# Performance work log

Measured on AMD Instinct MI355X. Metric: run time of the kernel, lower is better.

Reference implementation:

```python
import jax, jax.numpy as jnp
import numpy as np
from jax import lax

D_MODEL = 1024
D_STATE = 16
D_CONV = 4
D_INNER = 2048  # d_model * expand
B = 1
L = 1024


def setup_inputs() -> dict:
    key = jax.random.key(0)
    ks = jax.random.split(key, 8)
    nrm = lambda k, shape, s: jax.random.normal(k, shape, jnp.float32) * s
    x = nrm(ks[0], (B, L, D_MODEL), 1.0)
    in_proj_w = nrm(ks[1], (2 * D_INNER, D_MODEL), D_MODEL ** -0.5)
    conv_w = nrm(ks[2], (D_INNER, 1, D_CONV), D_CONV ** -0.5)
    conv_b = nrm(ks[3], (D_INNER,), 0.02)
    x_proj_w = nrm(ks[4], (D_INNER + 4 * D_STATE, D_INNER), D_INNER ** -0.5)
    # small dt so the log-cumsum-exp scan stays finite in fp32 over L steps
    dt_proj_w = nrm(ks[5], (D_INNER, D_INNER), 0.01 * D_INNER ** -0.5)
    dt_proj_b = jnp.full((D_INNER,), -6.0, jnp.float32)
    # faithful A_log init: real = -0.5*log(n), imag = pi*n
    n = np.arange(1, D_STATE + 1, dtype=np.float32)
    A_log_re = jnp.asarray(np.tile(np.log(n) * -0.5, (D_INNER, 1)))
    A_log_im = jnp.asarray(np.tile(np.pi * n, (D_INNER, 1)))
    D = jnp.ones((D_INNER,), jnp.float32)
    out_proj_w = nrm(ks[6], (D_MODEL, D_INNER), D_INNER ** -0.5)
    return dict(x=x, in_proj_w=in_proj_w, conv_w=conv_w, conv_b=conv_b,
                x_proj_w=x_proj_w, dt_proj_w=dt_proj_w, dt_proj_b=dt_proj_b,
                A_log_re=A_log_re, A_log_im=A_log_im, D=D, out_proj_w=out_proj_w)


def reference(x, in_proj_w, conv_w, conv_b, x_proj_w, dt_proj_w, dt_proj_b,
              A_log_re, A_log_im, D, out_proj_w):
    # input projection and gate split
    xz = x @ in_proj_w.T                          # (B, L, 2*d_inner)
    xc, z = jnp.split(xz, 2, axis=-1)
    # causal depthwise conv1d (torch pads both sides then truncates -> left pad only)
    xt = jnp.transpose(xc, (0, 2, 1))             # (B, d_inner, L)
    xp = jnp.pad(xt, ((0, 0), (0, 0), (D_CONV - 1, 0)))
    conv = lax.conv_general_dilated(
        xp, conv_w, window_strides=(1,), padding='VALID',
        dimension_numbers=('NCH', 'OIH', 'NCH'),
        feature_group_count=D_INNER) + conv_b[None, :, None]
    u = jnp.transpose(jax.nn.silu(conv), (0, 2, 1))  # (B, L, d_inner)
    # ssm parameter projection
    ssm = u @ x_proj_w.T                          # (B, L, d_inner + 4*d_state)
    delta = ssm[..., :D_INNER]
    B_re = ssm[..., D_INNER:D_INNER + D_STATE]
    B_im = ssm[..., D_INNER + D_STATE:D_INNER + 2 * D_STATE]
    C_re = ssm[..., D_INNER + 2 * D_STATE:D_INNER + 3 * D_STATE]
    C_im = ssm[..., D_INNER + 3 * D_STATE:]
    delta = jax.nn.softplus(delta @ dt_proj_w.T + dt_proj_b)  # (B, L, d_inner)
    Bc = (B_re + 1j * B_im).astype(jnp.complex64)             # (B, L, d_state)
    Cc = (C_re + 1j * C_im).astype(jnp.complex64)
    # complex selective scan via bilinear (Cayley) discretization + log-cumsum-exp
    A = -jnp.exp((A_log_re + 1j * A_log_im).astype(jnp.complex64))  # (d_inner, d_state)
    dt_c = delta[..., None].astype(jnp.complex64)             # (B, L, d_inner, 1)
    denom = 2.0 - dt_c * A                                    # (B, L, d_inner, d_state)
    numer = 2.0 + dt_c * A
    log_A_bar = jnp.log(numer) - jnp.log(denom)
    u_bar = (2.0 * dt_c / denom) * Bc[:, :, None, :] * u[..., None].astype(jnp.complex64)
    lc = jnp.cumsum(log_A_bar, axis=1)                        # cumulative log transition
    H = jnp.cumsum(jnp.exp(-lc) * u_bar, axis=1) * jnp.exp(lc)
    y = jnp.sum(Cc[:, :, None, :] * H, axis=-1).real + D * u  # (B, L, d_inner)
    y = y * jax.nn.silu(z)
    return y @ out_proj_w.T                                   # (B, L, d_model)
```

## Files before the change

kernel.cpp:

```cpp
#include <hip/hip_runtime.h>
#include <hip/hip_bf16.h>
#include <math.h>

#define L_SEQ   1024
#define DMODEL  1024
#define DINNER  2048
#define DSTATE  16
#define DCONV   4
#define NPROJ   (DINNER + 4 * DSTATE)
#define NCHUNK  16
#define CHUNK   64
#define NDN     (DINNER * DSTATE)

typedef __attribute__((ext_vector_type(8))) short  short8;
typedef __attribute__((ext_vector_type(8))) unsigned short us8;
typedef __attribute__((ext_vector_type(4))) float  f32x4;
typedef __attribute__((ext_vector_type(4))) unsigned short us4;

__device__ __forceinline__ float softplus_f(float v) {
    return fmaxf(v, 0.f) + log1pf(expf(-fabsf(v)));
}
__device__ __forceinline__ float silu_f(float v) {
    return v * __builtin_amdgcn_rcpf(1.f + expf(-v));
}

__device__ __forceinline__ void split1(float x, unsigned short& h, unsigned short& l) {
    unsigned b  = __float_as_uint(x);
    unsigned hb = b & 0xffff0000u;
    float    r  = x - __uint_as_float(hb);
    unsigned rb = __float_as_uint(r) + 0x8000u;
    h = (unsigned short)(hb >> 16);
    l = (unsigned short)(rb >> 16);
}
__device__ __forceinline__ void split4(float4 v, us4& h, us4& l) {
    float vv[4] = {v.x, v.y, v.z, v.w};
    #pragma unroll
    for (int i = 0; i < 4; ++i) {
        unsigned b  = __float_as_uint(vv[i]);
        unsigned hb = b & 0xffff0000u;
        float    r  = vv[i] - __uint_as_float(hb);
        unsigned rb = __float_as_uint(r) + 0x8000u;
        h[i] = (unsigned short)(hb >> 16);
        l[i] = (unsigned short)(rb >> 16);
    }
}

template<int BM>
__global__ __launch_bounds__(256) void gemm_mfma_sk(
    const float* __restrict__ A, const float* __restrict__ W,
    float* __restrict__ Cp, int M, int N, int K, int lda)
{
    constexpr int MF = BM / 32;
    constexpr int NF = 2;
    __shared__ unsigned short sAh[BM * 40], sAl[BM * 40];
    __shared__ unsigned short sBh[64 * 40], sBl[64 * 40];

    const int tid  = threadIdx.x;
    const int w    = tid >> 6;
    const int lane = tid & 63;
    const int wr   = w >> 1;
    const int wc   = w & 1;
    const int lrow = lane & 15;
    const int lkb  = lane >> 4;
    const int row0 = blockIdx.y * BM;
    const int col0 = blockIdx.x * 64;

    const int KS   = K / gridDim.z;
    const int kbeg = blockIdx.z * KS;
    const int kend = kbeg + KS;

    const int srow = tid >> 3;
    const int sfq  = tid & 7;

    f32x4 acc[MF][NF];
    #pragma unroll
    for (int m = 0; m < MF; ++m)
        #pragma unroll
        for (int n = 0; n < NF; ++n)
            acc[m][n] = (f32x4){0.f, 0.f, 0.f, 0.f};

    for (int k0 = kbeg; k0 < kend; k0 += 32) {
        #pragma unroll
        for (int p = 0; p < BM / 32; ++p) {
            int r = srow + p * 32;
            float4 v = *reinterpret_cast<const float4*>(
                A + (size_t)(row0 + r) * lda + k0 + sfq * 4);
            us4 h, l;
            split4(v, h, l);
            *reinterpret_cast<us4*>(sAh + r * 40 + sfq * 4) = h;
            *reinterpret_cast<us4*>(sAl + r * 40 + sfq * 4) = l;
        }
        #pragma unroll
        for (int p = 0; p < 2; ++p) {
            int r = srow + p * 32;
            float4 v = *reinterpret_cast<const float4*>(
                W + (size_t)(col0 + r) * K + k0 + sfq * 4);
            us4 h, l;
            split4(v, h, l);
            *reinterpret_cast<us4*>(sBh + r * 40 + sfq * 4) = h;
            *reinterpret_cast<us4*>(sBl + r * 40 + sfq * 4) = l;
        }
        __syncthreads();

        short8 ah[MF], al[MF], bh[NF], bl[NF];
        #pragma unroll
        for (int m = 0; m < MF; ++m) {
            int off = (wr * (BM / 2) + m * 16 + lrow) * 40 + lkb * 8;
            ah[m] = *reinterpret_cast<const short8*>(sAh + off);
            al[m] = *reinterpret_cast<const short8*>(sAl + off);
        }
        #pragma unroll
        for (int n = 0; n < NF; ++n) {
            int off = (wc * 32 + n * 16 + lrow) * 40 + lkb * 8;
            bh[n] = *reinterpret_cast<const short8*>(sBh + off);
            bl[n] = *reinterpret_cast<const short8*>(sBl + off);
        }

        #pragma unroll
        for (int m = 0; m < MF; ++m)
            #pragma unroll
            for (int n = 0; n < NF; ++n) {
                acc[m][n] = __builtin_amdgcn_mfma_f32_16x16x32_bf16(
                    ah[m], bh[n], acc[m][n], 0, 0, 0);
                acc[m][n] = __builtin_amdgcn_mfma_f32_16x16x32_bf16(
                    ah[m], bl[n], acc[m][n], 0, 0, 0);
                acc[m][n] = __builtin_amdgcn_mfma_f32_16x16x32_bf16(
                    al[m], bh[n], acc[m][n], 0, 0, 0);
            }
        __syncthreads();
    }

    float* Cb = Cp + (size_t)blockIdx.z * M * N;
    #pragma unroll
    for (int m = 0; m < MF; ++m)
        #pragma unroll
        for (int n = 0; n < NF; ++n) {
            int gr0 = row0 + wr * (BM / 2) + m * 16 + lkb * 4;
            int gc  = col0 + wc * 32 + n * 16 + lrow;
            #pragma unroll
            for (int r = 0; r < 4; ++r)
                Cb[(size_t)(gr0 + r) * N + gc] = acc[m][n][r];
        }
}

template<int BM>
__global__ __launch_bounds__(256) void gemm_bf16a_sk(
    const unsigned short* __restrict__ Ah, const unsigned short* __restrict__ Al,
    const float* __restrict__ W, float* __restrict__ Cp, int M, int N, int K)
{
    constexpr int MF = BM / 32;
    constexpr int NF = 2;
    constexpr int NL = BM / 64;
    __shared__ unsigned short sAh[BM * 40], sAl[BM * 40];
    __shared__ unsigned short sBh[64 * 40], sBl[64 * 40];

    const int tid  = threadIdx.x;
    const int w    = tid >> 6;
    const int lane = tid & 63;
    const int wr   = w >> 1;
    const int wc   = w & 1;
    const int lrow = lane & 15;
    const int lkb  = lane >> 4;
    const int row0 = blockIdx.y * BM;
    const int col0 = blockIdx.x * 64;

    const int KS   = K / gridDim.z;
    const int kbeg = blockIdx.z * KS;
    const int kend = kbeg + KS;

    const int srow = tid >> 3;
    const int sfq  = tid & 7;

    f32x4 acc[MF][NF];
    #pragma unroll
    for (int m = 0; m < MF; ++m)
        #pragma unroll
        for (int n = 0; n < NF; ++n)
            acc[m][n] = (f32x4){0.f, 0.f, 0.f, 0.f};

    for (int k0 = kbeg; k0 < kend; k0 += 32) {
        #pragma unroll
        for (int j = 0; j < NL; ++j) {
            int idx8 = j * 256 + tid;
            int r    = idx8 >> 2;
            int kq   = (idx8 & 3) * 8;
            size_t g = (size_t)(row0 + r) * K + k0 + kq;
            *reinterpret_cast<us8*>(sAh + r * 40 + kq) =
                *reinterpret_cast<const us8*>(Ah + g);
            *reinterpret_cast<us8*>(sAl + r * 40 + kq) =
                *reinterpret_cast<const us8*>(Al + g);
        }
        #pragma unroll
        for (int p = 0; p < 2; ++p) {
            int r = srow + p * 32;
            float4 v = *reinterpret_cast<const float4*>(
                W + (size_t)(col0 + r) * K + k0 + sfq * 4);
            us4 h, l;
            split4(v, h, l);
            *reinterpret_cast<us4*>(sBh + r * 40 + sfq * 4) = h;
            *reinterpret_cast<us4*>(sBl + r * 40 + sfq * 4) = l;
        }
        __syncthreads();

        short8 ah[MF], al[MF], bh[NF], bl[NF];
        #pragma unroll
        for (int m = 0; m < MF; ++m) {
            int off = (wr * (BM / 2) + m * 16 + lrow) * 40 + lkb * 8;
            ah[m] = *reinterpret_cast<const short8*>(sAh + off);
            al[m] = *reinterpret_cast<const short8*>(sAl + off);
        }
        #pragma unroll
        for (int n = 0; n < NF; ++n) {
            int off = (wc * 32 + n * 16 + lrow) * 40 + lkb * 8;
            bh[n] = *reinterpret_cast<const short8*>(sBh + off);
            bl[n] = *reinterpret_cast<const short8*>(sBl + off);
        }

        #pragma unroll
        for (int m = 0; m < MF; ++m)
            #pragma unroll
            for (int n = 0; n < NF; ++n) {
                acc[m][n] = __builtin_amdgcn_mfma_f32_16x16x32_bf16(
                    ah[m], bh[n], acc[m][n], 0, 0, 0);
                acc[m][n] = __builtin_amdgcn_mfma_f32_16x16x32_bf16(
                    ah[m], bl[n], acc[m][n], 0, 0, 0);
                acc[m][n] = __builtin_amdgcn_mfma_f32_16x16x32_bf16(
                    al[m], bh[n], acc[m][n], 0, 0, 0);
            }
        __syncthreads();
    }

    float* Cb = Cp + (size_t)blockIdx.z * M * N;
    #pragma unroll
    for (int m = 0; m < MF; ++m)
        #pragma unroll
        for (int n = 0; n < NF; ++n) {
            int gr0 = row0 + wr * (BM / 2) + m * 16 + lkb * 4;
            int gc  = col0 + wc * 32 + n * 16 + lrow;
            #pragma unroll
            for (int r = 0; r < 4; ++r)
                Cb[(size_t)(gr0 + r) * N + gc] = acc[m][n][r];
        }
}

template<int EPI, int SPLIT>
__global__ __launch_bounds__(256) void reduce_splitk(
    const float* __restrict__ part, float* __restrict__ out,
    const float* __restrict__ bias,
    unsigned short* __restrict__ oh, unsigned short* __restrict__ ol,
    int size, int N, int nsplit)
{
    int i = (blockIdx.x * 256 + threadIdx.x) * 4;
    if (i >= size) return;
    float4 s = *reinterpret_cast<const float4*>(part + i);
    for (int p = 1; p < nsplit; ++p) {
        float4 v = *reinterpret_cast<const float4*>(part + (size_t)p * size + i);
        s.x += v.x; s.y += v.y; s.z += v.z; s.w += v.w;
    }
    if (EPI == 1) {
        int col = i % N;
        float4 b = *reinterpret_cast<const float4*>(bias + col);
        s.x = softplus_f(s.x + b.x); s.y = softplus_f(s.y + b.y);
        s.z = softplus_f(s.z + b.z); s.w = softplus_f(s.w + b.w);
    }
    *reinterpret_cast<float4*>(out + i) = s;
    if (SPLIT == 1) {
        int col = i % N;
        if (col < 2048) {
            int row = i / N;
            us4 h, l;
            split4(s, h, l);
            *reinterpret_cast<us4*>(oh + (size_t)row * 2048 + col) = h;
            *reinterpret_cast<us4*>(ol + (size_t)row * 2048 + col) = l;
        }
    }
}

__global__ __launch_bounds__(256) void conv_silu_kernel(
    const float* __restrict__ xz, const float* __restrict__ cw,
    const float* __restrict__ cb, float* __restrict__ u,
    unsigned short* __restrict__ uh, unsigned short* __restrict__ ul)
{
    int idx = blockIdx.x * 256 + threadIdx.x;
    int l = idx >> 11;
    int d = idx & (DINNER - 1);
    float acc = cb[d];
    #pragma unroll
    for (int k = 0; k < DCONV; ++k) {
        int ls = l - (DCONV - 1) + k;
        float xv = (ls >= 0) ? xz[(size_t)ls * (2 * DINNER) + d] : 0.f;
        acc = fmaf(xv, cw[d * DCONV + k], acc);
    }
    float v = silu_f(acc);
    u[idx] = v;
    unsigned short h, lo;
    split1(v, h, lo);
    uh[idx] = h; ul[idx] = lo;
}

__device__ __forceinline__ void bilinear_coef(
    float dt, float a_re, float a_im,
    float& ab_re, float& ab_im, float& co_re, float& co_im)
{
    float dre = fmaf(-dt, a_re, 2.f);
    float dim = -dt * a_im;
    float inv = __builtin_amdgcn_rcpf(fmaf(dre, dre, dim * dim));
    float qre = dre * inv;
    float qim = -dim * inv;
    ab_re = fmaf(4.f, qre, -1.f);
    ab_im = 4.f * qim;
    float t2 = dt + dt;
    co_re = t2 * qre;
    co_im = t2 * qim;
}

__global__ __launch_bounds__(64) void scan_chunk_kernel(
    const float* __restrict__ delta, const float* __restrict__ ssm,
    const float* __restrict__ u,
    const float* __restrict__ A_log_re, const float* __restrict__ A_log_im,
    float2* __restrict__ Pc, float2* __restrict__ Sc)
{
    const int b = blockIdx.x;
    const int chunk = b >> 8;
    const int dg = b & 255;
    const int tid = threadIdx.x;
    const int n = tid & 15;
    const int dloc = tid >> 4;
    const int d0 = dg * 8 + dloc;
    const int d1 = d0 + 4;

    float m0 = expf(A_log_re[d0 * DSTATE + n]);
    float i0 = A_log_im[d0 * DSTATE + n];
    float a0r = -m0 * cosf(i0), a0i = -m0 * sinf(i0);
    float m1 = expf(A_log_re[d1 * DSTATE + n]);
    float i1 = A_log_im[d1 * DSTATE + n];
    float a1r = -m1 * cosf(i1), a1i = -m1 * sinf(i1);

    float p0r = 1.f, p0i = 0.f, s0r = 0.f, s0i = 0.f;
    float p1r = 1.f, p1i = 0.f, s1r = 0.f, s1i = 0.f;

    const int l0 = chunk * CHUNK;
    #pragma unroll 2
    for (int i = 0; i < CHUNK; ++i) {
        const int l = l0 + i;
        float dt0 = delta[(size_t)l * DINNER + d0];
        float dt1 = delta[(size_t)l * DINNER + d1];
        float uv0 = u[(size_t)l * DINNER + d0];
        float uv1 = u[(size_t)l * DINNER + d1];
        const float* srow = ssm + (size_t)l * NPROJ + DINNER;
        float br = srow[n];
        float bi = srow[DSTATE + n];

        float abr, abi, cor, coi;
        bilinear_coef(dt0, a0r, a0i, abr, abi, cor, coi);
        {
            float cbr = cor * br - coi * bi;
            float cbi = cor * bi + coi * br;
            float ur = cbr * uv0, ui = cbi * uv0;
            float sr = abr * s0r - abi * s0i + ur;
            float si = abr * s0i + abi * s0r + ui;
            s0r = sr; s0i = si;
            float pr = abr * p0r - abi * p0i;
            float pi = abr * p0i + abi * p0r;
            p0r = pr; p0i = pi;
        }
        bilinear_coef(dt1, a1r, a1i, abr, abi, cor, coi);
        {
            float cbr = cor * br - coi * bi;
            float cbi = cor * bi + coi * br;
            float ur = cbr * uv1, ui = cbi * uv1;
            float sr = abr * s1r - abi * s1i + ur;
            float si = abr * s1i + abi * s1r + ui;
            s1r = sr; s1i = si;
            float pr = abr * p1r - abi * p1i;
            float pi = abr * p1i + abi * p1r;
            p1r = pr; p1i = pi;
        }
    }

    int idx0 = chunk * NDN + d0 * DSTATE + n;
    int idx1 = chunk * NDN + d1 * DSTATE + n;
    Pc[idx0] = make_float2(p0r, p0i);
    Sc[idx0] = make_float2(s0r, s0i);
    Pc[idx1] = make_float2(p1r, p1i);
    Sc[idx1] = make_float2(s1r, s1i);
}

__global__ __launch_bounds__(256) void scan_combine_kernel(
    float2* __restrict__ Pc, const float2* __restrict__ Sc)
{
    const int td = blockIdx.x * 256 + threadIdx.x;
    float h_re = 0.f, h_im = 0.f;
    #pragma unroll
    for (int c = 0; c < NCHUNK; ++c) {
        float2 p = Pc[c * NDN + td];
        float2 s = Sc[c * NDN + td];
        Pc[c * NDN + td] = make_float2(h_re, h_im);
        float nr = s.x + p.x * h_re - p.y * h_im;
        float ni = s.y + p.x * h_im + p.y * h_re;
        h_re = nr; h_im = ni;
    }
}

__global__ __launch_bounds__(64) void scan_final_kernel(
    const float* __restrict__ delta, const float* __restrict__ ssm,
    const float* __restrict__ u, const float* __restrict__ xz,
    const float* __restrict__ A_log_re, const float* __restrict__ A_log_im,
    const float* __restrict__ Dvec, const float2* __restrict__ Hin,
    unsigned short* __restrict__ yh, unsigned short* __restrict__ yl)
{
    const int b = blockIdx.x;
    const int chunk = b >> 8;
    const int dg = b & 255;
    const int tid = threadIdx.x;
    const int n = tid & 15;
    const int dloc = tid >> 4;
    const int d0 = dg * 8 + dloc;
    const int d1 = d0 + 4;

    float m0 = expf(A_log_re[d0 * DSTATE + n]);
    float i0 = A_log_im[d0 * DSTATE + n];
    float a0r = -m0 * cosf(i0), a0i = -m0 * sinf(i0);
    float m1 = expf(A_log_re[d1 * DSTATE + n]);
    float i1 = A_log_im[d1 * DSTATE + n];
    float a1r = -m1 * cosf(i1), a1i = -m1 * sinf(i1);
    float Dd0 = Dvec[d0], Dd1 = Dvec[d1];

    float2 h0 = Hin[chunk * NDN + d0 * DSTATE + n];
    float2 h1 = Hin[chunk * NDN + d1 * DSTATE + n];
    float h0r = h0.x, h0i = h0.y, h1r = h1.x, h1i = h1.y;

    const int l0 = chunk * CHUNK;
    #pragma unroll 2
    for (int i = 0; i < CHUNK; ++i) {
        const int l = l0 + i;
        float dt0 = delta[(size_t)l * DINNER + d0];
        float dt1 = delta[(size_t)l * DINNER + d1];
        float uv0 = u[(size_t)l * DINNER + d0];
        float uv1 = u[(size_t)l * DINNER + d1];
        const float* srow = ssm + (size_t)l * NPROJ + DINNER;
        float br = srow[n];
        float bi = srow[DSTATE + n];
        float cr = srow[2 * DSTATE + n];
        float ci = srow[3 * DSTATE + n];

        float abr, abi, cor, coi;
        bilinear_coef(dt0, a0r, a0i, abr, abi, cor, coi);
        float c0;
        {
            float cbr = cor * br - coi * bi;
            float cbi = cor * bi + coi * br;
            float hr = abr * h0r - abi * h0i + cbr * uv0;
            float hi = abr * h0i + abi * h0r + cbi * uv0;
            h0r = hr; h0i = hi;
            c0 = cr * h0r - ci * h0i;
        }
        bilinear_coef(dt1, a1r, a1i, abr, abi, cor, coi);
        float c1;
        {
            float cbr = cor * br - coi * bi;
            float cbi = cor * bi + coi * br;
            float hr = abr * h1r - abi * h1i + cbr * uv1;
            float hi = abr * h1i + abi * h1r + cbi * uv1;
            h1r = hr; h1i = hi;
            c1 = cr * h1r - ci * h1i;
        }
        c0 += __shfl_xor(c0, 1, 16);
        c0 += __shfl_xor(c0, 2, 16);
        c0 += __shfl_xor(c0, 4, 16);
        c0 += __shfl_xor(c0, 8, 16);
        c1 += __shfl_xor(c1, 1, 16);
        c1 += __shfl_xor(c1, 2, 16);
        c1 += __shfl_xor(c1, 4, 16);
        c1 += __shfl_xor(c1, 8, 16);
        if (n == 0) {
            float zv0 = xz[(size_t)l * (2 * DINNER) + DINNER + d0];
            float zv1 = xz[(size_t)l * (2 * DINNER) + DINNER + d1];
            float o0 = (c0 + Dd0 * uv0) * silu_f(zv0);
            float o1 = (c1 + Dd1 * uv1) * silu_f(zv1);
            unsigned short hh, ll;
            split1(o0, hh, ll);
            yh[(size_t)l * DINNER + d0] = hh; yl[(size_t)l * DINNER + d0] = ll;
            split1(o1, hh, ll);
            yh[(size_t)l * DINNER + d1] = hh; yl[(size_t)l * DINNER + d1] = ll;
        }
    }
}

extern "C" void kernel_launch(void* const* d_in, const int* in_sizes, int n_in,
                              void* d_out, int out_size, void* d_ws, size_t ws_size,
                              hipStream_t stream)
{
    const float* x         = (const float*)d_in[0];
    const float* in_proj_w = (const float*)d_in[1];
    const float* conv_w    = (const float*)d_in[2];
    const float* conv_b    = (const float*)d_in[3];
    const float* x_proj_w  = (const float*)d_in[4];
    const float* dt_proj_w = (const float*)d_in[5];
    const float* dt_proj_b = (const float*)d_in[6];
    const float* A_log_re  = (const float*)d_in[7];
    const float* A_log_im  = (const float*)d_in[8];
    const float* Dvec      = (const float*)d_in[9];
    const float* out_proj_w= (const float*)d_in[10];
    float* out = (float*)d_out;

    float* ws    = (float*)d_ws;
    float* xz    = ws;
    float* u     = xz    + (size_t)L_SEQ * 2 * DINNER;
    float* ssm   = u     + (size_t)L_SEQ * DINNER;
    float* delta = ssm   + (size_t)L_SEQ * NPROJ;
    float2* Pc   = (float2*)(delta + (size_t)L_SEQ * DINNER);
    float2* Sc   = Pc + (size_t)NCHUNK * NDN;
    float* part  = (float*)(Sc + (size_t)NCHUNK * NDN);
    unsigned short* uh = (unsigned short*)(part + (size_t)4 * L_SEQ * NPROJ);
    unsigned short* ul = uh + (size_t)L_SEQ * DINNER;
    unsigned short* sh = ul + (size_t)L_SEQ * DINNER;
    unsigned short* sl = sh + (size_t)L_SEQ * DINNER;
    unsigned short* yh = sl + (size_t)L_SEQ * DINNER;
    unsigned short* yl = yh + (size_t)L_SEQ * DINNER;

    gemm_mfma_sk<128><<<dim3((2 * DINNER) / 64, L_SEQ / 128, 2), 256, 0, stream>>>(
        x, in_proj_w, part, L_SEQ, 2 * DINNER, DMODEL, DMODEL);
    reduce_splitk<0, 0><<<(L_SEQ * 2 * DINNER) / 1024, 256, 0, stream>>>(
        part, xz, nullptr, nullptr, nullptr, L_SEQ * 2 * DINNER, 2 * DINNER, 2);

    conv_silu_kernel<<<(L_SEQ * DINNER) / 256, 256, 0, stream>>>(
        xz, conv_w, conv_b, u, uh, ul);

    gemm_bf16a_sk<128><<<dim3(NPROJ / 64, L_SEQ / 128, 4), 256, 0, stream>>>(
        uh, ul, x_proj_w, part, L_SEQ, NPROJ, DINNER);
    reduce_splitk<0, 1><<<(L_SEQ * NPROJ) / 1024, 256, 0, stream>>>(
        part, ssm, nullptr, sh, sl, L_SEQ * NPROJ, NPROJ, 4);

    gemm_bf16a_sk<128><<<dim3(DINNER / 64, L_SEQ / 128, 4), 256, 0, stream>>>(
        sh, sl, dt_proj_w, part, L_SEQ, DINNER, DINNER);
    reduce_splitk<1, 0><<<(L_SEQ * DINNER) / 1024, 256, 0, stream>>>(
        part, delta, dt_proj_b, nullptr, nullptr, L_SEQ * DINNER, DINNER, 4);

    scan_chunk_kernel<<<(DINNER / 8) * NCHUNK, 64, 0, stream>>>(
        delta, ssm, u, A_log_re, A_log_im, Pc, Sc);
    scan_combine_kernel<<<NDN / 256, 256, 0, stream>>>(Pc, Sc);
    scan_final_kernel<<<(DINNER / 8) * NCHUNK, 64, 0, stream>>>(
        delta, ssm, u, xz, A_log_re, A_log_im, Dvec, Pc, yh, yl);

    gemm_bf16a_sk<64><<<dim3(DMODEL / 64, L_SEQ / 64, 4), 256, 0, stream>>>(
        yh, yl, out_proj_w, part, L_SEQ, DMODEL, DINNER);
    reduce_splitk<0, 0><<<(L_SEQ * DMODEL) / 1024, 256, 0, stream>>>(
        part, out, nullptr, nullptr, nullptr, L_SEQ * DMODEL, DMODEL, 4);
}
```

Before: 438.6 us.

## Pre-split inputs and weights to bf16 hi/lo once, halve scan per-thread work

Adds a split kernel that converts x and all four weight matrices to bf16 hi/lo arrays in the workspace at the start of each call. A new GEMM variant then loads both operands as pre-split bf16, so the per-tile fp32 load and split of the weight tiles (repeated by every row-block) goes away. The scan kernels are also changed to one channel per thread group with twice as many blocks, giving more parallelism but the same per-block latency chain. The cost is extra launches and a full fp32 read plus bf16 write of every weight each call, and the fast path needs a larger workspace (it falls back otherwise).

```diff
diff --git a/kernel.cpp b/kernel.cpp
--- a/kernel.cpp
+++ b/kernel.cpp
@@ -45,13 +45,27 @@
     }
 }
 
+__global__ __launch_bounds__(256) void split_kernel(
+    const float* __restrict__ in, unsigned short* __restrict__ h,
+    unsigned short* __restrict__ l)
+{
+    int i = (blockIdx.x * 256 + threadIdx.x) * 4;
+    float4 v = *reinterpret_cast<const float4*>(in + i);
+    us4 hh, ll;
+    split4(v, hh, ll);
+    *reinterpret_cast<us4*>(h + i) = hh;
+    *reinterpret_cast<us4*>(l + i) = ll;
+}
+
 template<int BM>
-__global__ __launch_bounds__(256) void gemm_mfma_sk(
-    const float* __restrict__ A, const float* __restrict__ W,
-    float* __restrict__ Cp, int M, int N, int K, int lda)
-{
-    constexpr int MF = BM / 32;
-    constexpr int NF = 2;
+__global__ __launch_bounds__(256) void gemm_bf16ab_sk(
+    const unsigned short* __restrict__ Ah, const unsigned short* __restrict__ Al,
+    const unsigned short* __restrict__ Wh, const unsigned short* __restrict__ Wl,
+    float* __restrict__ Cp, int M, int N, int K)
+{
+    constexpr int MF  = BM / 32;
+    constexpr int NF  = 2;
+    constexpr int NLA = BM / 64;
     __shared__ unsigned short sAh[BM * 40], sAl[BM * 40];
     __shared__ unsigned short sBh[64 * 40], sBl[64 * 40];
 
@@ -69,9 +83,6 @@
     const int kbeg = blockIdx.z * KS;
     const int kend = kbeg + KS;
 
-    const int srow = tid >> 3;
-    const int sfq  = tid & 7;
-
     f32x4 acc[MF][NF];
     #pragma unroll
     for (int m = 0; m < MF; ++m)
@@ -79,26 +90,27 @@
         for (int n = 0; n < NF; ++n)
             acc[m][n] = (f32x4){0.f, 0.f, 0.f, 0.f};
 
+    const int wrow = tid >> 2;
+    const int wkq  = (tid & 3) * 8;
+
     for (int k0 = kbeg; k0 < kend; k0 += 32) {
         #pragma unroll
-        for (int p = 0; p < BM / 32; ++p) {
-            int r = srow + p * 32;
-            float4 v = *reinterpret_cast<const float4*>(
-                A + (size_t)(row0 + r) * lda + k0 + sfq * 4);
-            us4 h, l;
-            split4(v, h, l);
-            *reinterpret_cast<us4*>(sAh + r * 40 + sfq * 4) = h;
-            *reinterpret_cast<us4*>(sAl + r * 40 + sfq * 4) = l;
-        }
-        #pragma unroll
-        for (int p = 0; p < 2; ++p) {
-            int r = srow + p * 32;
-            float4 v = *reinterpret_cast<const float4*>(
-                W + (size_t)(col0 + r) * K + k0 + sfq * 4);
-            us4 h, l;
-            split4(v, h, l);
-            *reinterpret_cast<us4*>(sBh + r * 40 + sfq * 4) = h;
-            *reinterpret_cast<us4*>(sBl + r * 40 + sfq * 4) = l;
+        for (int j = 0; j < NLA; ++j) {
+            int idx8 = j * 256 + tid;
+            int r    = idx8 >> 2;
+            int kq   = (idx8 & 3) * 8;
+            size_t g = (size_t)(row0 + r) * K + k0 + kq;
+            *reinterpret_cast<us8*>(sAh + r * 40 + kq) =
+                *reinterpret_cast<const us8*>(Ah + g);
+            *reinterpret_cast<us8*>(sAl + r * 40 + kq) =
+                *reinterpret_cast<const us8*>(Al + g);
+        }
+        {
+            size_t g = (size_t)(col0 + wrow) * K + k0 + wkq;
+            *reinterpret_cast<us8*>(sBh + wrow * 40 + wkq) =
+                *reinterpret_cast<const us8*>(Wh + g);
+            *reinterpret_cast<us8*>(sBl + wrow * 40 + wkq) =
+                *reinterpret_cast<const us8*>(Wl + g);
         }
         __syncthreads();
 
@@ -144,16 +156,14 @@
 }
 
 template<int BM>
-__global__ __launch_bounds__(256) void gemm_bf16a_sk(
-    const unsigned short* __restrict__ Ah, const unsigned short* __restrict__ Al,
-    const float* __restrict__ W, float* __restrict__ Cp, int M, int N, int K)
+__global__ __launch_bounds__(256) void gemm_mfma_sk(
+    const float* __restrict__ A, const float* __restrict__ W,
+    float* __restrict__ Cp, int M, int N, int K, int lda)
 {
     constexpr int MF = BM / 32;
     constexpr int NF = 2;
-    constexpr int NL = BM / 64;
     __shared__ unsigned short sAh[BM * 40], sAl[BM * 40];
     __shared__ unsigned short sBh[64 * 40], sBl[64 * 40];
-
     const int tid  = threadIdx.x;
     const int w    = tid >> 6;
     const int lane = tid & 63;
@@ -163,11 +173,102 @@
     const int lkb  = lane >> 4;
     const int row0 = blockIdx.y * BM;
     const int col0 = blockIdx.x * 64;
-
     const int KS   = K / gridDim.z;
     const int kbeg = blockIdx.z * KS;
     const int kend = kbeg + KS;
-
+    const int srow = tid >> 3;
+    const int sfq  = tid & 7;
+
+    f32x4 acc[MF][NF];
+    #pragma unroll
+    for (int m = 0; m < MF; ++m)
+        #pragma unroll
+        for (int n = 0; n < NF; ++n)
+            acc[m][n] = (f32x4){0.f, 0.f, 0.f, 0.f};
+
+    for (int k0 = kbeg; k0 < kend; k0 += 32) {
+        #pragma unroll
+        for (int p = 0; p < BM / 32; ++p) {
+            int r = srow + p * 32;
+            float4 v = *reinterpret_cast<const float4*>(
+                A + (size_t)(row0 + r) * lda + k0 + sfq * 4);
+            us4 h, l;
+            split4(v, h, l);
+            *reinterpret_cast<us4*>(sAh + r * 40 + sfq * 4) = h;
+            *reinterpret_cast<us4*>(sAl + r * 40 + sfq * 4) = l;
+        }
+        #pragma unroll
+        for (int p = 0; p < 2; ++p) {
+            int r = srow + p * 32;
+            float4 v = *reinterpret_cast<const float4*>(
+                W + (size_t)(col0 + r) * K + k0 + sfq * 4);
+            us4 h, l;
+            split4(v, h, l);
+            *reinterpret_cast<us4*>(sBh + r * 40 + sfq * 4) = h;
+            *reinterpret_cast<us4*>(sBl + r * 40 + sfq * 4) = l;
+        }
+        __syncthreads();
+        short8 ah[MF], al[MF], bh[NF], bl[NF];
+        #pragma unroll
+        for (int m = 0; m < MF; ++m) {
+            int off = (wr * (BM / 2) + m * 16 + lrow) * 40 + lkb * 8;
+            ah[m] = *reinterpret_cast<const short8*>(sAh + off);
+            al[m] = *reinterpret_cast<const short8*>(sAl + off);
+        }
+        #pragma unroll
+        for (int n = 0; n < NF; ++n) {
+            int off = (wc * 32 + n * 16 + lrow) * 40 + lkb * 8;
+            bh[n] = *reinterpret_cast<const short8*>(sBh + off);
+            bl[n] = *reinterpret_cast<const short8*>(sBl + off);
+        }
+        #pragma unroll
+        for (int m = 0; m < MF; ++m)
+            #pragma unroll
+            for (int n = 0; n < NF; ++n) {
+                acc[m][n] = __builtin_amdgcn_mfma_f32_16x16x32_bf16(
+                    ah[m], bh[n], acc[m][n], 0, 0, 0);
+                acc[m][n] = __builtin_amdgcn_mfma_f32_16x16x32_bf16(
+                    ah[m], bl[n], acc[m][n], 0, 0, 0);
+                acc[m][n] = __builtin_amdgcn_mfma_f32_16x16x32_bf16(
+                    al[m], bh[n], acc[m][n], 0, 0, 0);
+            }
+        __syncthreads();
+    }
+    float* Cb = Cp + (size_t)blockIdx.z * M * N;
+    #pragma unroll
+    for (int m = 0; m < MF; ++m)
+        #pragma unroll
+        for (int n = 0; n < NF; ++n) {
+            int gr0 = row0 + wr * (BM / 2) + m * 16 + lkb * 4;
+            int gc  = col0 + wc * 32 + n * 16 + lrow;
+            #pragma unroll
+            for (int r = 0; r < 4; ++r)
+                Cb[(size_t)(gr0 + r) * N + gc] = acc[m][n][r];
+        }
+}
+
+template<int BM>
+__global__ __launch_bounds__(256) void gemm_bf16a_sk(
+    const unsigned short* __restrict__ Ah, const unsigned short* __restrict__ Al,
+    const float* __restrict__ W, float* __restrict__ Cp, int M, int N, int K)
+{
+    constexpr int MF = BM / 32;
+    constexpr int NF = 2;
+    constexpr int NL = BM / 64;
+    __shared__ unsigned short sAh[BM * 40], sAl[BM * 40];
+    __shared__ unsigned short sBh[64 * 40], sBl[64 * 40];
+    const int tid  = threadIdx.x;
+    const int w    = tid >> 6;
+    const int lane = tid & 63;
+    const int wr   = w >> 1;
+    const int wc   = w & 1;
+    const int lrow = lane & 15;
+    const int lkb  = lane >> 4;
+    const int row0 = blockIdx.y * BM;
+    const int col0 = blockIdx.x * 64;
+    const int KS   = K / gridDim.z;
+    const int kbeg = blockIdx.z * KS;
+    const int kend = kbeg + KS;
     const int srow = tid >> 3;
     const int sfq  = tid & 7;
 
@@ -201,7 +302,6 @@
             *reinterpret_cast<us4*>(sBl + r * 40 + sfq * 4) = l;
         }
         __syncthreads();
-
         short8 ah[MF], al[MF], bh[NF], bl[NF];
         #pragma unroll
         for (int m = 0; m < MF; ++m) {
@@ -215,7 +315,6 @@
             bh[n] = *reinterpret_cast<const short8*>(sBh + off);
             bl[n] = *reinterpret_cast<const short8*>(sBl + off);
         }
-
         #pragma unroll
         for (int m = 0; m < MF; ++m)
             #pragma unroll
@@ -229,7 +328,6 @@
             }
         __syncthreads();
     }
-
     float* Cb = Cp + (size_t)blockIdx.z * M * N;
     #pragma unroll
     for (int m = 0; m < MF; ++m)
@@ -321,69 +419,49 @@
     float2* __restrict__ Pc, float2* __restrict__ Sc)
 {
     const int b = blockIdx.x;
-    const int chunk = b >> 8;
-    const int dg = b & 255;
+    const int chunk = b >> 9;
+    const int d4 = b & 511;
     const int tid = threadIdx.x;
     const int n = tid & 15;
     const int dloc = tid >> 4;
-    const int d0 = dg * 8 + dloc;
-    const int d1 = d0 + 4;
-
-    float m0 = expf(A_log_re[d0 * DSTATE + n]);
-    float i0 = A_log_im[d0 * DSTATE + n];
-    float a0r = -m0 * cosf(i0), a0i = -m0 * sinf(i0);
-    float m1 = expf(A_log_re[d1 * DSTATE + n]);
-    float i1 = A_log_im[d1 * DSTATE + n];
-    float a1r = -m1 * cosf(i1), a1i = -m1 * sinf(i1);
-
-    float p0r = 1.f, p0i = 0.f, s0r = 0.f, s0i = 0.f;
-    float p1r = 1.f, p1i = 0.f, s1r = 0.f, s1i = 0.f;
+    const int d = d4 * 4 + dloc;
+
+    const float mag  = expf(A_log_re[d * DSTATE + n]);
+    const float alim = A_log_im[d * DSTATE + n];
+    const float a_re = -mag * cosf(alim);
+    const float a_im = -mag * sinf(alim);
+
+    float p_re = 1.f, p_im = 0.f;
+    float s_re = 0.f, s_im = 0.f;
 
     const int l0 = chunk * CHUNK;
-    #pragma unroll 2
+    #pragma unroll 4
     for (int i = 0; i < CHUNK; ++i) {
         const int l = l0 + i;
-        float dt0 = delta[(size_t)l * DINNER + d0];
-        float dt1 = delta[(size_t)l * DINNER + d1];
-        float uv0 = u[(size_t)l * DINNER + d0];
-        float uv1 = u[(size_t)l * DINNER + d1];
+        float dt = delta[(size_t)l * DINNER + d];
+        float uv = u[(size_t)l * DINNER + d];
         const float* srow = ssm + (size_t)l * NPROJ + DINNER;
         float br = srow[n];
         float bi = srow[DSTATE + n];
 
-        float abr, abi, cor, coi;
-        bilinear_coef(dt0, a0r, a0i, abr, abi, cor, coi);
-        {
-            float cbr = cor * br - coi * bi;
-            float cbi = cor * bi + coi * br;
-            float ur = cbr * uv0, ui = cbi * uv0;
-            float sr = abr * s0r - abi * s0i + ur;
-            float si = abr * s0i + abi * s0r + ui;
-            s0r = sr; s0i = si;
-            float pr = abr * p0r - abi * p0i;
-            float pi = abr * p0i + abi * p0r;
-            p0r = pr; p0i = pi;
-        }
-        bilinear_coef(dt1, a1r, a1i, abr, abi, cor, coi);
-        {
-            float cbr = cor * br - coi * bi;
-            float cbi = cor * bi + coi * br;
-            float ur = cbr * uv1, ui = cbi * uv1;
-            float sr = abr * s1r - abi * s1i + ur;
-            float si = abr * s1i + abi * s1r + ui;
-            s1r = sr; s1i = si;
-            float pr = abr * p1r - abi * p1i;
-            float pi = abr * p1i + abi * p1r;
-            p1r = pr; p1i = pi;
-        }
-    }
-
-    int idx0 = chunk * NDN + d0 * DSTATE + n;
-    int idx1 = chunk * NDN + d1 * DSTATE + n;
-    Pc[idx0] = make_float2(p0r, p0i);
-    Sc[idx0] = make_float2(s0r, s0i);
-    Pc[idx1] = make_float2(p1r, p1i);
-    Sc[idx1] = make_float2(s1r, s1i);
+        float ab_re, ab_im, co_re, co_im;
+        bilinear_coef(dt, a_re, a_im, ab_re, ab_im, co_re, co_im);
+        float cbr = co_re * br - co_im * bi;
+        float cbi = co_re * bi + co_im * br;
+        float ub_re = cbr * uv;
+        float ub_im = cbi * uv;
+
+        float sr = ab_re * s_re - ab_im * s_im + ub_re;
+        float si = ab_re * s_im + ab_im * s_re + ub_im;
+        s_re = sr; s_im = si;
+        float pr = ab_re * p_re - ab_im * p_im;
+        float pi = ab_re * p_im + ab_im * p_re;
+        p_re = pr; p_im = pi;
+    }
+
+    const int idx = chunk * NDN + d * DSTATE + n;
+    Pc[idx] = make_float2(p_re, p_im);
+    Sc[idx] = make_float2(s_re, s_im);
 }
 
 __global__ __launch_bounds__(256) void scan_combine_kernel(
@@ -410,79 +488,55 @@
     unsigned short* __restrict__ yh, unsigned short* __restrict__ yl)
 {
     const int b = blockIdx.x;
-    const int chunk = b >> 8;
-    const int dg = b & 255;
+    const int chunk = b >> 9;
+    const int d4 = b & 511;
     const int tid = threadIdx.x;
     const int n = tid & 15;
     const int dloc = tid >> 4;
-    const int d0 = dg * 8 + dloc;
-    const int d1 = d0 + 4;
-
-    float m0 = expf(A_log_re[d0 * DSTATE + n]);
-    float i0 = A_log_im[d0 * DSTATE + n];
-    float a0r = -m0 * cosf(i0), a0i = -m0 * sinf(i0);
-    float m1 = expf(A_log_re[d1 * DSTATE + n]);
-    float i1 = A_log_im[d1 * DSTATE + n];
-    float a1r = -m1 * cosf(i1), a1i = -m1 * sinf(i1);
-    float Dd0 = Dvec[d0], Dd1 = Dvec[d1];
-
-    float2 h0 = Hin[chunk * NDN + d0 * DSTATE + n];
-    float2 h1 = Hin[chunk * NDN + d1 * DSTATE + n];
-    float h0r = h0.x, h0i = h0.y, h1r = h1.x, h1i = h1.y;
+    const int d = d4 * 4 + dloc;
+
+    const float mag  = expf(A_log_re[d * DSTATE + n]);
+    const float alim = A_log_im[d * DSTATE + n];
+    const float a_re = -mag * cosf(alim);
+    const float a_im = -mag * sinf(alim);
+    const float Dd   = Dvec[d];
+
+    float2 h0 = Hin[chunk * NDN + d * DSTATE + n];
+    float h_re = h0.x, h_im = h0.y;
 
     const int l0 = chunk * CHUNK;
     #pragma unroll 2
     for (int i = 0; i < CHUNK; ++i) {
         const int l = l0 + i;
-        float dt0 = delta[(size_t)l * DINNER + d0];
-        float dt1 = delta[(size_t)l * DINNER + d1];
-        float uv0 = u[(size_t)l * DINNER + d0];
-        float uv1 = u[(size_t)l * DINNER + d1];
+        float dt = delta[(size_t)l * DINNER + d];
+        float uv = u[(size_t)l * DINNER + d];
         const float* srow = ssm + (size_t)l * NPROJ + DINNER;
         float br = srow[n];
         float bi = srow[DSTATE + n];
         float cr = srow[2 * DSTATE + n];
         float ci = srow[3 * DSTATE + n];
 
-        float abr, abi, cor, coi;
-        bilinear_coef(dt0, a0r, a0i, abr, abi, cor, coi);
-        float c0;
-        {
-            float cbr = cor * br - coi * bi;
-            float cbi = cor * bi + coi * br;
-            float hr = abr * h0r - abi * h0i + cbr * uv0;
-            float hi = abr * h0i + abi * h0r + cbi * uv0;
-            h0r = hr; h0i = hi;
-            c0 = cr * h0r - ci * h0i;
-        }
-        bilinear_coef(dt1, a1r, a1i, abr, abi, cor, coi);
-        float c1;
-        {
-            float cbr = cor * br - coi * bi;
-            float cbi = cor * bi + coi * br;
-            float hr = abr * h1r - abi * h1i + cbr * uv1;
-            float hi = abr * h1i + abi * h1r + cbi * uv1;
-            h1r = hr; h1i = hi;
-            c1 = cr * h1r - ci * h1i;
-        }
-        c0 += __shfl_xor(c0, 1, 16);
-        c0 += __shfl_xor(c0, 2, 16);
-        c0 += __shfl_xor(c0, 4, 16);
-        c0 += __shfl_xor(c0, 8, 16);
-        c1 += __shfl_xor(c1, 1, 16);
-        c1 += __shfl_xor(c1, 2, 16);
-        c1 += __shfl_xor(c1, 4, 16);
-        c1 += __shfl_xor(c1, 8, 16);
+        float ab_re, ab_im, co_re, co_im;
+        bilinear_coef(dt, a_re, a_im, ab_re, ab_im, co_re, co_im);
+        float cbr = co_re * br - co_im * bi;
+        float cbi = co_re * bi + co_im * br;
+
+        float hr = ab_re * h_re - ab_im * h_im + cbr * uv;
+        float hi = ab_re * h_im + ab_im * h_re + cbi * uv;
+        h_re = hr; h_im = hi;
+
+        float contrib = cr * h_re - ci * h_im;
+        contrib += __shfl_xor(contrib, 1, 16);
+        contrib += __shfl_xor(contrib, 2, 16);
+        contrib += __shfl_xor(contrib, 4, 16);
+        contrib += __shfl_xor(contrib, 8, 16);
         if (n == 0) {
-            float zv0 = xz[(size_t)l * (2 * DINNER) + DINNER + d0];
-            float zv1 = xz[(size_t)l * (2 * DINNER) + DINNER + d1];
-            float o0 = (c0 + Dd0 * uv0) * silu_f(zv0);
-            float o1 = (c1 + Dd1 * uv1) * silu_f(zv1);
+            float zv = xz[(size_t)l * (2 * DINNER) + DINNER + d];
+            float o = (contrib + Dd * uv) * silu_f(zv);
             unsigned short hh, ll;
-            split1(o0, hh, ll);
-            yh[(size_t)l * DINNER + d0] = hh; yl[(size_t)l * DINNER + d0] = ll;
-            split1(o1, hh, ll);
-            yh[(size_t)l * DINNER + d1] = hh; yl[(size_t)l * DINNER + d1] = ll;
+            split1(o, hh, ll);
+            yh[(size_t)l * DINNER + d] = hh;
+            yl[(size_t)l * DINNER + d] = ll;
         }
     }
 }
@@ -518,33 +572,72 @@
     unsigned short* sl = sh + (size_t)L_SEQ * DINNER;
     unsigned short* yh = sl + (size_t)L_SEQ * DINNER;
     unsigned short* yl = yh + (size_t)L_SEQ * DINNER;
-
-    gemm_mfma_sk<128><<<dim3((2 * DINNER) / 64, L_SEQ / 128, 2), 256, 0, stream>>>(
-        x, in_proj_w, part, L_SEQ, 2 * DINNER, DMODEL, DMODEL);
+    unsigned short* xh  = yl  + (size_t)L_SEQ * DINNER;
+    unsigned short* xl  = xh  + (size_t)L_SEQ * DMODEL;
+    unsigned short* w1h = xl  + (size_t)L_SEQ * DMODEL;
+    unsigned short* w1l = w1h + (size_t)2 * DINNER * DMODEL;
+    unsigned short* w3h = w1l + (size_t)2 * DINNER * DMODEL;
+    unsigned short* w3l = w3h + (size_t)NPROJ * DINNER;
+    unsigned short* w4h = w3l + (size_t)NPROJ * DINNER;
+    unsigned short* w4l = w4h + (size_t)DINNER * DINNER;
+    unsigned short* w6h = w4l + (size_t)DINNER * DINNER;
+    unsigned short* w6l = w6h + (size_t)DMODEL * DINNER;
+    const size_t NEED = ((size_t)(w6l + (size_t)DMODEL * DINNER - (unsigned short*)ws)) * 2;
+
+    const bool pre = (ws_size >= NEED);
+
+    if (pre) {
+        split_kernel<<<(L_SEQ * DMODEL) / 1024, 256, 0, stream>>>(x, xh, xl);
+        split_kernel<<<(2 * DINNER * DMODEL) / 1024, 256, 0, stream>>>(in_proj_w, w1h, w1l);
+        split_kernel<<<(NPROJ * DINNER) / 1024, 256, 0, stream>>>(x_proj_w, w3h, w3l);
+        split_kernel<<<(DINNER * DINNER) / 1024, 256, 0, stream>>>(dt_proj_w, w4h, w4l);
+        split_kernel<<<(DMODEL * DINNER) / 1024, 256, 0, stream>>>(out_proj_w, w6h, w6l);
+
+        gemm_bf16ab_sk<128><<<dim3((2 * DINNER) / 64, L_SEQ / 128, 2), 256, 0, stream>>>(
+            xh, xl, w1h, w1l, part, L_SEQ, 2 * DINNER, DMODEL);
+    } else {
+        gemm_mfma_sk<128><<<dim3((2 * DINNER) / 64, L_SEQ / 128, 2), 256, 0, stream>>>(
+            x, in_proj_w, part, L_SEQ, 2 * DINNER, DMODEL, DMODEL);
+    }
     reduce_splitk<0, 0><<<(L_SEQ * 2 * DINNER) / 1024, 256, 0, stream>>>(
         part, xz, nullptr, nullptr, nullptr, L_SEQ * 2 * DINNER, 2 * DINNER, 2);
 
     conv_silu_kernel<<<(L_SEQ * DINNER) / 256, 256, 0, stream>>>(
         xz, conv_w, conv_b, u, uh, ul);
 
-    gemm_bf16a_sk<128><<<dim3(NPROJ / 64, L_SEQ / 128, 4), 256, 0, stream>>>(
-        uh, ul, x_proj_w, part, L_SEQ, NPROJ, DINNER);
+    if (pre) {
+        gemm_bf16ab_sk<128><<<dim3(NPROJ / 64, L_SEQ / 128, 4), 256, 0, stream>>>(
+            uh, ul, w3h, w3l, part, L_SEQ, NPROJ, DINNER);
+    } else {
+        gemm_bf16a_sk<128><<<dim3(NPROJ / 64, L_SEQ / 128, 4), 256, 0, stream>>>(
+            uh, ul, x_proj_w, part, L_SEQ, NPROJ, DINNER);
+    }
     reduce_splitk<0, 1><<<(L_SEQ * NPROJ) / 1024, 256, 0, stream>>>(
         part, ssm, nullptr, sh, sl, L_SEQ * NPROJ, NPROJ, 4);
 
-    gemm_bf16a_sk<128><<<dim3(DINNER / 64, L_SEQ / 128, 4), 256, 0, stream>>>(
-        sh, sl, dt_proj_w, part, L_SEQ, DINNER, DINNER);
+    if (pre) {
+        gemm_bf16ab_sk<128><<<dim3(DINNER / 64, L_SEQ / 128, 4), 256, 0, stream>>>(
+            sh, sl, w4h, w4l, part, L_SEQ, DINNER, DINNER);
+    } else {
+        gemm_bf16a_sk<128><<<dim3(DINNER / 64, L_SEQ / 128, 4), 256, 0, stream>>>(
+            sh, sl, dt_proj_w, part, L_SEQ, DINNER, DINNER);
+    }
     reduce_splitk<1, 0><<<(L_SEQ * DINNER) / 1024, 256, 0, stream>>>(
         part, delta, dt_proj_b, nullptr, nullptr, L_SEQ * DINNER, DINNER, 4);
 
-    scan_chunk_kernel<<<(DINNER / 8) * NCHUNK, 64, 0, stream>>>(
+    scan_chunk_kernel<<<(DINNER / 4) * NCHUNK, 64, 0, stream>>>(
         delta, ssm, u, A_log_re, A_log_im, Pc, Sc);
     scan_combine_kernel<<<NDN / 256, 256, 0, stream>>>(Pc, Sc);
-    scan_final_kernel<<<(DINNER / 8) * NCHUNK, 64, 0, stream>>>(
+    scan_final_kernel<<<(DINNER / 4) * NCHUNK, 64, 0, stream>>>(
         delta, ssm, u, xz, A_log_re, A_log_im, Dvec, Pc, yh, yl);
 
-    gemm_bf16a_sk<64><<<dim3(DMODEL / 64, L_SEQ / 64, 4), 256, 0, stream>>>(
-        yh, yl, out_proj_w, part, L_SEQ, DMODEL, DINNER);
+    if (pre) {
+        gemm_bf16ab_sk<64><<<dim3(DMODEL / 64, L_SEQ / 64, 4), 256, 0, stream>>>(
+            yh, yl, w6h, w6l, part, L_SEQ, DMODEL, DINNER);
+    } else {
+        gemm_bf16a_sk<64><<<dim3(DMODEL / 64, L_SEQ / 64, 4), 256, 0, stream>>>(
+            yh, yl, out_proj_w, part, L_SEQ, DMODEL, DINNER);
+    }
     reduce_splitk<0, 0><<<(L_SEQ * DMODEL) / 1024, 256, 0, stream>>>(
         part, out, nullptr, nullptr, nullptr, L_SEQ * DMODEL, DMODEL, 4);
 }
```

Result: faster. 429.2 us (-2.1%).
